# Performance work log

Measured on AMD Instinct MI355X. Metric: run time of the kernel, lower is better.

The kernel has to match this reference:

```python
import jax, jax.numpy as jnp
import numpy as np

B, Q, K, D, H = 2, 1024, 4096, 1024, 16
DH = D // H
LN_EPS = 1e-5


def setup_inputs() -> dict:
    key = jax.random.key(0)
    ks = jax.random.split(key, 10)
    queries = jax.random.normal(ks[0], (B, Q, D), jnp.float32)
    keys = jax.random.normal(ks[1], (B, K, D), jnp.float32)
    values = jax.random.normal(ks[2], (B, K, D), jnp.float32)
    # 128 words of 8 query tokens each: boundaries 0,8,...,1024 (sorted, unique)
    word_boundaries = jnp.arange(0, Q + 1, 8, dtype=jnp.int32)  # [129]
    # monotone map from query positions to char/key positions in [0, K]
    char_boundaries = jnp.sort(jax.random.randint(ks[3], (Q,), 0, K + 1, dtype=jnp.int32))
    s = 0.02
    ln_gamma = jnp.ones((D,), jnp.float32)
    ln_beta = jnp.zeros((D,), jnp.float32)
    in_proj_w = jax.random.normal(ks[4], (3 * D, D), jnp.float32) * s
    in_proj_b = jnp.zeros((3 * D,), jnp.float32)
    out_w = jax.random.normal(ks[5], (D, D), jnp.float32) * s
    out_b = jnp.zeros((D,), jnp.float32)
    return dict(queries=queries, keys=keys, values=values,
                word_boundaries=word_boundaries, char_boundaries=char_boundaries,
                ln_gamma=ln_gamma, ln_beta=ln_beta,
                in_proj_w=in_proj_w, in_proj_b=in_proj_b,
                out_w=out_w, out_b=out_b)


def char_aware_mask(wb, cb, q_len, k_len):
    """Vectorized version of the per-word python loop.
    Float mask of 0/1 (PyTorch ADDS a float attn_mask to the scores)."""
    ws, we = wb[:-1], wb[1:]                     # word start/end in query coords [nW]
    nW = ws.shape[0]
    cs = cb[ws]                                  # char span start per word
    ce = cb[we - 1]                              # char span end per word
    q = jnp.arange(q_len)
    i = jnp.clip(jnp.searchsorted(wb, q, side='right') - 1, 0, nW - 1)  # word id per query row
    valid = (q >= ws[i]) & (q < we[i])           # rows actually written by the loop
    j = jnp.arange(k_len)[None, :]               # [1, K]
    in_char = (j >= cs[i][:, None]) & (j < ce[i][:, None])
    # prev word: keys [wb[i-1], wb[i]) (query-coord indices used on key axis, as in source)
    ps = ws[jnp.maximum(i - 1, 0)]
    in_prev = (i > 0)[:, None] & (j >= ps[:, None]) & (j < ws[i][:, None])
    # next word: keys [wb[i+1], wb[i+2])
    ns = we[i]
    ne = wb[jnp.minimum(i + 2, nW)]
    in_next = (i < nW - 1)[:, None] & (j >= ns[:, None]) & (j < ne[:, None])
    return (valid[:, None] & (in_char | in_prev | in_next)).astype(jnp.float32)


def reference(queries, keys, values, word_boundaries, char_boundaries,
              ln_gamma, ln_beta, in_proj_w, in_proj_b, out_w, out_b):
    b, q_len, d = queries.shape
    k_len = keys.shape[1]
    mask = char_aware_mask(word_boundaries, char_boundaries, q_len, k_len)  # [Q, K]
    # LayerNorm(queries)
    mu = jnp.mean(queries, axis=-1, keepdims=True)
    var = jnp.var(queries, axis=-1, keepdims=True)
    x = (queries - mu) * jax.lax.rsqrt(var + LN_EPS) * ln_gamma + ln_beta
    # MultiheadAttention(x, keys, values, attn_mask=mask) -- float mask added to logits
    wq, wk, wv = jnp.split(in_proj_w, 3, axis=0)
    bq, bk, bv = jnp.split(in_proj_b, 3)
    qh = (x @ wq.T + bq).reshape(b, q_len, H, DH)
    kh = (keys @ wk.T + bk).reshape(b, k_len, H, DH)
    vh = (values @ wv.T + bv).reshape(b, k_len, H, DH)
    scale = 1.0 / jnp.sqrt(jnp.asarray(DH, queries.dtype))
    scores = jnp.einsum('bqhd,bkhd->bhqk', qh * scale, kh) + mask[None, None]
    attn = jax.nn.softmax(scores, axis=-1)
    ctx = jnp.einsum('bhqk,bkhd->bqhd', attn, vh).reshape(b, q_len, d)
    out = ctx @ out_w.T + out_b
    # residual; dropout is identity at inference
    return queries + out
```

## Files before the change

### kernel.cpp

```cpp
#include <hip/hip_runtime.h>
#include <hip/hip_bf16.h>


typedef __attribute__((ext_vector_type(8))) short bf16x8;
typedef __attribute__((ext_vector_type(4))) float f32x4;
typedef __attribute__((ext_vector_type(16))) float f32x16;

#define L2E 1.44269504088896341f
#define CSCALE (0.125f * L2E)
#define NSPLIT 4

__device__ __forceinline__ short f2bf(float f) {
  __hip_bfloat16 h = __float2bfloat16(f);
  return reinterpret_cast<short&>(h);
}

__device__ __forceinline__ unsigned cvtpk(float a, float b) {
  unsigned r;
  asm("v_cvt_pk_bf16_f32 %0, %1, %2" : "=v"(r) : "v"(a), "v"(b));
  return r;
}

__device__ __forceinline__ float fexp2(float x) {
#if __has_builtin(__builtin_amdgcn_exp2f)
  return __builtin_amdgcn_exp2f(x);
#else
  float r;
  asm("v_exp_f32 %0, %1" : "=v"(r) : "v"(x));
  return r;
#endif
}

__device__ __forceinline__ void halfswap(unsigned a, unsigned b, unsigned& x, unsigned& y) {
#if __has_builtin(__builtin_amdgcn_permlane32_swap)
  auto r = __builtin_amdgcn_permlane32_swap(a, b, false, false);
  x = (unsigned)r[0];
  y = (unsigned)r[1];
#else
  unsigned ca = (unsigned)__shfl_xor((int)a, 32);
  unsigned cb = (unsigned)__shfl_xor((int)b, 32);
  bool h = ((threadIdx.x & 63) >> 5) != 0;
  x = h ? cb : a;
  y = h ? b : ca;
#endif
}

__device__ __forceinline__ void gload16(const void* g, void* l) {
  __builtin_amdgcn_global_load_lds(
      (const __attribute__((address_space(1))) void*)g,
      (__attribute__((address_space(3))) void*)l, 16, 0, 0);
}

__device__ __forceinline__ void bar() { __builtin_amdgcn_s_barrier(); }

template <int N>
__device__ __forceinline__ void vmbar() {
  if constexpr (N == 8)
    asm volatile("s_waitcnt vmcnt(8)" ::: "memory");
  else
    asm volatile("s_waitcnt vmcnt(0)" ::: "memory");
  __builtin_amdgcn_s_barrier();
}

__device__ __forceinline__ void lgkm0() {
  asm volatile("s_waitcnt lgkmcnt(0)" ::: "memory");
  __builtin_amdgcn_sched_barrier(0);
}

__device__ __forceinline__ void ivcalc(int q, const int* __restrict__ wb,
                                       const int* __restrict__ cb, int* p) {
  int cnt = 0;
  for (int k = 0; k < 129; ++k) cnt += (wb[k] <= q) ? 1 : 0;
  int i = cnt - 1;
  i = i < 0 ? 0 : (i > 127 ? 127 : i);
  bool valid = (q >= wb[i]) && (q < wb[i + 1]);
  p[0] = p[1] = p[2] = p[3] = p[4] = p[5] = 0;
  if (valid) {
    p[0] = cb[wb[i]];
    p[1] = cb[wb[i + 1] - 1];
    if (i > 0) { p[2] = wb[i - 1]; p[3] = wb[i]; }
    if (i < 127) { p[4] = wb[i + 1]; p[5] = wb[(i + 2 <= 128) ? i + 2 : 128]; }
  }
}

__device__ __forceinline__ unsigned inrange3(int key, const int* p) {
  bool m = (key >= p[0] && key < p[1]) || (key >= p[2] && key < p[3]) ||
           (key >= p[4] && key < p[5]);
  return m ? 1u : 0u;
}

__global__ __launch_bounds__(256) void prep_kernel(const float* __restrict__ w,
                                                   const float* __restrict__ o,
                                                   short* __restrict__ dw,
                                                   short* __restrict__ dof,
                                                   const float* __restrict__ x,
                                                   const float* __restrict__ gamma,
                                                   const float* __restrict__ beta,
                                                   short* __restrict__ xout,
                                                   const int* __restrict__ wb,
                                                   const int* __restrict__ cb,
                                                   uint4* __restrict__ pmf,
                                                   const float* __restrict__ keys,
                                                   const float* __restrict__ values,
                                                   short* __restrict__ kbf,
                                                   short* __restrict__ vbf) {
  const int blk = blockIdx.x;
  const int t = threadIdx.x;
  if (blk < 2048) {
    int base = blk * 256 + t;
#pragma unroll
    for (int i = 0; i < 10; ++i) {
      long f = (long)base + (long)i * 524288;
      const float* s;
      short* d;
      if (f < 786432) {
        long e = f * 4;
        s = w + e; d = dw + e;
      } else if (f < 1048576) {
        long e = (f - 786432) * 4;
        s = o + e; d = dof + e;
      } else if (f < 3145728) {
        long e = (f - 1048576) * 4;
        s = keys + e; d = kbf + e;
      } else {
        long e = (f - 3145728) * 4;
        s = values + e; d = vbf + e;
      }
      float4 xv = *(const float4*)s;
      uint2 r;
      r.x = cvtpk(xv.x, xv.y);
      r.y = cvtpk(xv.z, xv.w);
      *(uint2*)d = r;
    }
  } else if (blk < 4096) {
    const int row = blk - 2048;
    float4 v = ((const float4*)(x + (size_t)row * 1024))[t];
    float s = v.x + v.y + v.z + v.w;
    float ss = v.x * v.x + v.y * v.y + v.z * v.z + v.w * v.w;
#pragma unroll
    for (int d = 32; d; d >>= 1) { s += __shfl_xor(s, d); ss += __shfl_xor(ss, d); }
    __shared__ float red[8];
    int wv2 = t >> 6, lane = t & 63;
    if (lane == 0) { red[wv2] = s; red[4 + wv2] = ss; }
    __syncthreads();
    s = red[0] + red[1] + red[2] + red[3];
    ss = red[4] + red[5] + red[6] + red[7];
    float mean = s * (1.0f / 1024.0f);
    float var = ss * (1.0f / 1024.0f) - mean * mean;
    float rstd = rsqrtf(var + 1e-5f);
    float4 g = ((const float4*)gamma)[t];
    float4 b = ((const float4*)beta)[t];
    uint2 oo;
    oo.x = cvtpk((v.x - mean) * rstd * g.x + b.x, (v.y - mean) * rstd * g.y + b.y);
    oo.y = cvtpk((v.z - mean) * rstd * g.z + b.z, (v.w - mean) * rstd * g.w + b.w);
    ((uint2*)(xout + (size_t)row * 1024))[t] = oo;
  } else {
    __shared__ int ivs[16][6];
    int mb = blk - 4096;
    if (t < 16) {
      int wg = (mb * 4 + (t >> 2)) & 31;
      int q = wg * 32 + (t & 3) * 8;
      ivcalc(q, wb, cb, ivs[t]);
    }
    __syncthreads();
    int idx = mb * 256 + t;
    int lane = idx & 63;
    int g4 = t >> 6;
    int tt = idx >> 11;
    int l31 = lane & 31, hi = lane >> 5;
    uint4 oo = {0u, 0u, 0u, 0u};
    if (!hi) {
      const int* p0 = ivs[g4 * 4 + 0];
      const int* p1 = ivs[g4 * 4 + 1];
      const int* p2 = ivs[g4 * 4 + 2];
      const int* p3 = ivs[g4 * 4 + 3];
      int key0 = tt * 64 + l31, key1 = key0 + 32;
      unsigned b0 = inrange3(key0, p0), b1 = inrange3(key0, p1);
      unsigned b2 = inrange3(key0, p2), b3 = inrange3(key0, p3);
      oo.x = (b0 | (b1 << 16)) * 0x3F80u;
      oo.y = (b2 | (b3 << 16)) * 0x3F80u;
      b0 = inrange3(key1, p0); b1 = inrange3(key1, p1);
      b2 = inrange3(key1, p2); b3 = inrange3(key1, p3);
      oo.z = (b0 | (b1 << 16)) * 0x3F80u;
      oo.w = (b2 | (b3 << 16)) * 0x3F80u;
    }
    pmf[idx] = oo;
  }
}

__device__ __forceinline__ void kv256_body(short* lds, const short* __restrict__ Agl,
                                           const short* __restrict__ Bgl,
                                           const float* __restrict__ bias,
                                           short* __restrict__ Cout, int mode,
                                           int bx, int by) {
  const int tid = (int)threadIdx.x;
  const int lane = tid & 63;
  const int w = tid >> 6;
  const int wm = w >> 2, wn = w & 3;
  const int l16 = lane & 15, lhi = lane >> 4;
  const int gc8 = (lane & 7) ^ (lane >> 3);
  const int lr = lane >> 3;
  const int rsw = (l16 & 7) << 4;
  const int m0 = bx * 256, n0 = by * 256;

  f32x4 acc[8][4];
#pragma unroll
  for (int i = 0; i < 8; ++i)
#pragma unroll
    for (int j = 0; j < 4; ++j) acc[i][j] = f32x4{0.f, 0.f, 0.f, 0.f};

  auto SU = [&](int k, int unit) {
    const int k0 = k * 64;
    short* base = lds + (k & 1) * 32768;
#pragma unroll
    for (int j = 0; j < 2; ++j) {
      int i = w * 2 + j;
      int ch;
      bool isA;
      if (unit == 1)      { ch = (i < 8) ? i : i + 8;       isA = true; }
      else if (unit == 4) { ch = 8 + ((i < 8) ? i : i + 8); isA = true; }
      else if (unit == 2) { ch = (i >> 2) * 8 + (i & 3);    isA = false; }
      else                { ch = 4 + (i >> 2) * 8 + (i & 3); isA = false; }
      const short* g = isA ? (Agl + (size_t)(m0 + ch * 8 + lr) * 1024 + k0 + gc8 * 8)
                           : (Bgl + (size_t)(n0 + ch * 8 + lr) * 1024 + k0 + gc8 * 8);
      gload16(g, base + (isA ? 0 : 16384) + ch * 512);
    }
  };

  bf16x8 af[4][2], b0[2][2], b1[2][2];
  auto LDA = [&](int bsel, int qm) {
    const char* cA = (const char*)(lds + bsel * 32768);
#pragma unroll
    for (int mt = 0; mt < 4; ++mt)
#pragma unroll
      for (int kk = 0; kk < 2; ++kk) {
        int row = wm * 128 + qm * 64 + mt * 16 + l16;
        af[mt][kk] = *(const bf16x8*)(cA + row * 128 + ((kk * 64 + lhi * 16) ^ rsw));
      }
  };
  auto LDB = [&](int bsel, int qn, bf16x8 (&bf)[2][2]) {
    const char* cB = (const char*)(lds + bsel * 32768) + 32768;
#pragma unroll
    for (int nt = 0; nt < 2; ++nt)
#pragma unroll
      for (int kk = 0; kk < 2; ++kk) {
        int row = wn * 64 + qn * 32 + nt * 16 + l16;
        bf[nt][kk] = *(const bf16x8*)(cB + row * 128 + ((kk * 64 + lhi * 16) ^ rsw));
      }
  };
  auto MM = [&](int qm, int qn, bf16x8 (&bf)[2][2]) {
    __builtin_amdgcn_s_setprio(1);
#pragma unroll
    for (int kk = 0; kk < 2; ++kk)
#pragma unroll
      for (int mt = 0; mt < 4; ++mt)
#pragma unroll
        for (int nt = 0; nt < 2; ++nt)
          acc[qm * 4 + mt][qn * 2 + nt] = __builtin_amdgcn_mfma_f32_16x16x32_bf16(
              af[mt][kk], bf[nt][kk], acc[qm * 4 + mt][qn * 2 + nt], 0, 0, 0);
    __builtin_amdgcn_s_setprio(0);
  };

  SU(0, 1); SU(0, 2); SU(0, 3); SU(0, 4);
  SU(1, 1); SU(1, 2); SU(1, 3); SU(1, 4);
  vmbar<8>();

#pragma unroll 2
  for (int k = 0; k < 14; ++k) {
    const int bs = k & 1;
    LDA(bs, 0); LDB(bs, 0, b0);
    lgkm0(); MM(0, 0, b0); bar();
    LDB(bs, 1, b1); SU(k + 2, 1);
    lgkm0(); MM(0, 1, b1); bar();
    LDA(bs, 1); SU(k + 2, 2);
    lgkm0(); MM(1, 0, b0); bar();
    SU(k + 2, 3); SU(k + 2, 4);
    MM(1, 1, b1);
    vmbar<8>();
  }
  {
    LDA(0, 0); LDB(0, 0, b0);
    lgkm0(); MM(0, 0, b0);
    LDB(0, 1, b1);
    lgkm0(); MM(0, 1, b1);
    LDA(0, 1);
    lgkm0(); MM(1, 0, b0);
    MM(1, 1, b1);
    vmbar<0>();
  }
  {
    LDA(1, 0); LDB(1, 0, b0);
    lgkm0(); MM(0, 0, b0);
    LDB(1, 1, b1);
    lgkm0(); MM(0, 1, b1);
    LDA(1, 1);
    lgkm0(); MM(1, 0, b0);
    MM(1, 1, b1);
  }

#pragma unroll
  for (int mt = 0; mt < 8; ++mt)
#pragma unroll
    for (int nt = 0; nt < 4; ++nt) {
      int n = n0 + wn * 64 + nt * 16 + l16;
#pragma unroll
      for (int r = 0; r < 4; ++r) {
        int m = m0 + wm * 128 + mt * 16 + lhi * 4 + r;
        float v = acc[mt][nt][r];
        if (mode == 0) {
          int bb = m >> 12, key = m & 4095;
          int hh = n >> 6, dhl = n & 63;
          Cout[((size_t)((bb * 16 + hh) * 4096 + key)) * 64 + dhl] = f2bf(v + bias[n]);
        } else {
          int bb = n >> 12, key = n & 4095;
          Cout[((size_t)(bb * 1024 + m)) * 4096 + key] = f2bf(v + bias[m]);
        }
      }
    }
}

__device__ __forceinline__ void gemmQO_body(short* lA, short* lB,
                                            const short* __restrict__ A,
                                            const short* __restrict__ W,
                                            const float* __restrict__ bias,
                                            const float* __restrict__ resid,
                                            void* __restrict__ Cout, int mode,
                                            float scale, int bxi, int byi) {
  const int lane = threadIdx.x & 63;
  const int w = threadIdx.x >> 6;
  const int m0 = bxi * 64;
  const int n0 = byi * 128;
  const int wm = w >> 2, wn = w & 3;
  const int l16 = lane & 15, lhi = lane >> 4;

  const int gc8 = (lane & 7) ^ (lane >> 3);
  const int lr = lane >> 3;
  const int rsw = (l16 & 7) << 4;

  f32x4 zero = {0.f, 0.f, 0.f, 0.f};
  f32x4 acc[2][2];
#pragma unroll
  for (int i = 0; i < 2; ++i)
#pragma unroll
    for (int j = 0; j < 2; ++j) acc[i][j] = zero;

  for (int k0 = 0; k0 < 1024; k0 += 64) {
    __syncthreads();
#pragma unroll
    for (int j = 0; j < 3; ++j) {
      int c = w * 3 + j;
      if (c < 8)
        gload16(A + (size_t)(m0 + c * 8 + lr) * 1024 + k0 + gc8 * 8, &lA[c * 512]);
      else
        gload16(W + (size_t)(n0 + (c - 8) * 8 + lr) * 1024 + k0 + gc8 * 8,
                &lB[(c - 8) * 512]);
    }
    __syncthreads();
    bf16x8 af[2][2], bfr[2][2];
#pragma unroll
    for (int mt = 0; mt < 2; ++mt)
#pragma unroll
      for (int kk = 0; kk < 2; ++kk)
        af[mt][kk] = *(const bf16x8*)((const char*)lA + (wm * 32 + mt * 16 + l16) * 128 +
                                      ((kk * 64 + lhi * 16) ^ rsw));
#pragma unroll
    for (int nt = 0; nt < 2; ++nt)
#pragma unroll
      for (int kk = 0; kk < 2; ++kk)
        bfr[nt][kk] = *(const bf16x8*)((const char*)lB + (wn * 32 + nt * 16 + l16) * 128 +
                                       ((kk * 64 + lhi * 16) ^ rsw));
#pragma unroll
    for (int kk = 0; kk < 2; ++kk)
#pragma unroll
      for (int mt = 0; mt < 2; ++mt)
#pragma unroll
        for (int nt = 0; nt < 2; ++nt)
          acc[mt][nt] = __builtin_amdgcn_mfma_f32_16x16x32_bf16(af[mt][kk], bfr[nt][kk],
                                                                acc[mt][nt], 0, 0, 0);
  }

#pragma unroll
  for (int mt = 0; mt < 2; ++mt)
#pragma unroll
    for (int nt = 0; nt < 2; ++nt) {
      int col = n0 + wn * 32 + nt * 16 + l16;
      float bs = bias[col];
#pragma unroll
      for (int r = 0; r < 4; ++r) {
        int row = m0 + wm * 32 + mt * 16 + lhi * 4 + r;
        float v = acc[mt][nt][r] + bs;
        if (mode == 0) {
          ((short*)Cout)[(size_t)row * 1024 + col] = f2bf(v * scale);
        } else {
          size_t idx = (size_t)row * 1024 + col;
          ((float*)Cout)[idx] = v + resid[idx];
        }
      }
    }
}

__global__ __launch_bounds__(512, 2) void megaGemm_kernel(const short* __restrict__ kbf,
                                                          const short* __restrict__ wk,
                                                          const float* __restrict__ kbias,
                                                          const short* __restrict__ wv,
                                                          const short* __restrict__ vbf,
                                                          const float* __restrict__ vbias,
                                                          short* __restrict__ khp,
                                                          short* __restrict__ vhT,
                                                          const short* __restrict__ xb,
                                                          const short* __restrict__ wq,
                                                          const float* __restrict__ qbias,
                                                          short* __restrict__ qhb) {
  __shared__ __attribute__((aligned(16))) short lds[65536];
  int id = blockIdx.x;
  if (id < 128) {
    kv256_body(lds, kbf, wk, kbias, khp, 0, id & 31, id >> 5);
  } else if (id < 256) {
    int i2 = id & 127;
    kv256_body(lds, wv, vbf, vbias, vhT, 1, i2 >> 5, i2 & 31);
  } else {
    int i2 = id - 256;
    gemmQO_body(lds, lds + 4096, xb, wq, qbias, nullptr, qhb, 0, CSCALE, i2 & 31, i2 >> 5);
  }
}

__global__ __launch_bounds__(512, 4) void gemmQO_kernel(const short* __restrict__ A,
                                                        const short* __restrict__ W,
                                                        const float* __restrict__ bias,
                                                        const float* __restrict__ resid,
                                                        void* __restrict__ Cout, int mode,
                                                        float scale) {
  __shared__ __attribute__((aligned(16))) short lA[4096];
  __shared__ __attribute__((aligned(16))) short lB[8192];
  gemmQO_body(lA, lB, A, W, bias, resid, Cout, mode, scale, blockIdx.x, blockIdx.y);
}

__global__ __launch_bounds__(256, 4) void attn15_kernel(const short* __restrict__ qh,
                                                        const short* __restrict__ khp,
                                                        const short* __restrict__ vtp,
                                                        const uint4* __restrict__ pmf,
                                                        short* __restrict__ pacc,
                                                        float* __restrict__ pml) {
  const int tid = threadIdx.x;
  const int lane = tid & 63;
  const int w = tid >> 6;
  const int l31 = lane & 31;
  const int hi = lane >> 5;
  const int id = blockIdx.x;
  const int qb = id >> 7;
  const int g = id & 127;
  const int bh = g >> 2;
  const int ks = g & 3;
  const int b = bh >> 4, h = bh & 15;

  __shared__ __attribute__((aligned(16))) short sK[2][4096];
  __shared__ __attribute__((aligned(16))) short sV[2][4096];

  const int wq0 = qb * 128 + w * 32;
  const int qrow = wq0 + l31;
  bf16x8 qf0, qf1, qf2, qf3;
  {
    const short* qp = qh + ((size_t)(b * 1024 + qrow)) * 1024 + h * 64 + hi * 8;
    qf0 = *(const bf16x8*)(qp);
    qf1 = *(const bf16x8*)(qp + 16);
    qf2 = *(const bf16x8*)(qp + 32);
    qf3 = *(const bf16x8*)(qp + 48);
  }

  bf16x8 bmv;
  {
    union { unsigned u[4]; bf16x8 v; } t;
    t.u[0] = t.u[1] = t.u[2] = t.u[3] = 0;
    int lj = l31 >> 3;
    unsigned val = 0x3FB9u << (16 * (lj & 1));
    if (!hi) t.u[lj >> 1] = val;
    bmv = t.v;
  }

  f32x16 fzero;
#pragma unroll
  for (int i = 0; i < 16; ++i) fzero[i] = 0.f;

  const int kchunk = ks * 1024;
  const int sub = (lane & 7) ^ (lane >> 3);
  const int r8 = lane >> 3;
  const size_t kbase_g = ((size_t)bh * 4096 + kchunk) * 64;
  const size_t vbase_g = ((size_t)bh * 64) * 4096 + (size_t)kchunk;
  const uint4* pmfp = pmf + ((size_t)(ks * 16) * 32 + qb * 4 + w) * 64 + lane;

  f32x16 acc0, acc1;
#pragma unroll
  for (int i = 0; i < 16; ++i) { acc0[i] = 0.f; acc1[i] = 0.f; }
  float rs = 0.f;

  const int koff_swz = ((lane & 7) ^ ((lane >> 3) & 3)) << 4;

  auto STAGE = [&](int buf, int t) {
    int kt = t * 64;
#pragma unroll
    for (int q2 = 0; q2 < 2; ++q2) {
      int ch = w * 2 + q2;
      int sub2 = sub ^ (ch & 3);
      gload16(khp + kbase_g + (size_t)(kt + ch * 8 + r8) * 64 + sub2 * 8,
              (short*)sK[buf] + ch * 512);
      gload16(vtp + vbase_g + (size_t)(ch * 8 + r8) * 4096 + kt + sub2 * 8,
              (short*)sV[buf] + ch * 512);
    }
  };

  auto HALF = [&](int buf, unsigned mlo, unsigned mhi, int rowb, bf16x8& paA, bf16x8& paB) {
    bf16x8 am;
    {
      union { unsigned u[4]; bf16x8 v; } f;
      f.u[0] = mlo; f.u[1] = mhi; f.u[2] = 0; f.u[3] = 0;
      am = f.v;
    }
    __builtin_amdgcn_s_setprio(1);
    f32x16 ss = __builtin_amdgcn_mfma_f32_32x32x16_bf16(am, bmv, fzero, 0, 0, 0);
#pragma unroll
    for (int c = 0; c < 4; ++c) {
      int off = (c * 32 + hi * 16) ^ koff_swz;
      bf16x8 k0 = *(const bf16x8*)((const char*)sK[buf] + (rowb + l31) * 128 + off);
      bf16x8 qc = (c == 0) ? qf0 : (c == 1) ? qf1 : (c == 2) ? qf2 : qf3;
      ss = __builtin_amdgcn_mfma_f32_32x32x16_bf16(k0, qc, ss, 0, 0, 0);
    }
    __builtin_amdgcn_s_setprio(0);
#pragma unroll
    for (int r = 0; r < 16; ++r) ss[r] = fexp2(ss[r]);
    {
      float t0 = ss[0] + ss[1], t1 = ss[2] + ss[3], t2 = ss[4] + ss[5], t3 = ss[6] + ss[7];
      float t4 = ss[8] + ss[9], t5 = ss[10] + ss[11], t6 = ss[12] + ss[13],
            t7 = ss[14] + ss[15];
      rs += ((t0 + t1) + (t2 + t3)) + ((t4 + t5) + (t6 + t7));
    }
    unsigned a01 = cvtpk(ss[0], ss[1]), a23 = cvtpk(ss[2], ss[3]);
    unsigned a45 = cvtpk(ss[4], ss[5]), a67 = cvtpk(ss[6], ss[7]);
    unsigned a89 = cvtpk(ss[8], ss[9]), aAB = cvtpk(ss[10], ss[11]);
    unsigned aCD = cvtpk(ss[12], ss[13]), aEF = cvtpk(ss[14], ss[15]);
    union { unsigned u[4]; bf16x8 v; } f;
    halfswap(a01, a45, f.u[0], f.u[2]);
    halfswap(a23, a67, f.u[1], f.u[3]);
    paA = f.v;
    halfswap(a89, aCD, f.u[0], f.u[2]);
    halfswap(aAB, aEF, f.u[1], f.u[3]);
    paB = f.v;
  };

  uint4 mf_cur = pmfp[0];
  uint4 mf_next = mf_cur;
  STAGE(0, 0);
  __syncthreads();
  int buf = 0;

  for (int t = 0; t < 16; ++t) {
    if (t < 15) {
      STAGE(buf ^ 1, t + 1);
      mf_next = pmfp[(size_t)(t + 1) * 2048];
    }

    bf16x8 pa0, pa1, pa2, pa3;
    HALF(buf, mf_cur.x, mf_cur.y, 0, pa0, pa1);
    HALF(buf, mf_cur.z, mf_cur.w, 32, pa2, pa3);

    __builtin_amdgcn_s_setprio(1);
#pragma unroll
    for (int kb16 = 0; kb16 < 4; ++kb16) {
      int off = (kb16 * 32 + hi * 16) ^ koff_swz;
      bf16x8 v0 = *(const bf16x8*)((const char*)sV[buf] + l31 * 128 + off);
      bf16x8 v1 = *(const bf16x8*)((const char*)sV[buf] + (32 + l31) * 128 + off);
      bf16x8 pa = (kb16 == 0) ? pa0 : (kb16 == 1) ? pa1 : (kb16 == 2) ? pa2 : pa3;
      acc0 = __builtin_amdgcn_mfma_f32_32x32x16_bf16(pa, v0, acc0, 0, 0, 0);
      acc1 = __builtin_amdgcn_mfma_f32_32x32x16_bf16(pa, v1, acc1, 0, 0, 0);
    }
    __builtin_amdgcn_s_setprio(0);
    __syncthreads();
    buf ^= 1;
    mf_cur = mf_next;
  }

  short* paccp = pacc + (((size_t)ks * 32 + bh) * 1024) * 64;
#pragma unroll
  for (int r = 0; r < 16; r += 2) {
    int q0 = wq0 + ((r & 3) + 8 * (r >> 2)) + 4 * hi;
    int q1 = wq0 + (((r + 1) & 3) + 8 * ((r + 1) >> 2)) + 4 * hi;
    unsigned u0 = cvtpk(acc0[r], acc0[r + 1]);
    unsigned u1 = cvtpk(acc1[r], acc1[r + 1]);
    paccp[(size_t)q0 * 64 + l31] = (short)(u0 & 0xffffu);
    paccp[(size_t)q1 * 64 + l31] = (short)(u0 >> 16);
    paccp[(size_t)q0 * 64 + 32 + l31] = (short)(u1 & 0xffffu);
    paccp[(size_t)q1 * 64 + 32 + l31] = (short)(u1 >> 16);
  }
  rs += __shfl_xor(rs, 32);
  if (hi == 0) {
    float* mlp = pml + ((size_t)ks * 32 + bh) * 1024;
    mlp[wq0 + l31] = rs;
  }
}

__global__ __launch_bounds__(256) void combine_kernel(const short* __restrict__ pacc,
                                                      const float* __restrict__ pml,
                                                      short* __restrict__ ctx) {
  int idx = blockIdx.x * 256 + threadIdx.x;
  int dh8 = idx & 7;
  int row = idx >> 3;
  int bh = row >> 10, q = row & 1023;
  float L = 0.f;
  float o0 = 0.f, o1 = 0.f, o2 = 0.f, o3 = 0.f, o4 = 0.f, o5 = 0.f, o6 = 0.f, o7 = 0.f;
#pragma unroll
  for (int k = 0; k < NSPLIT; ++k) {
    L += pml[((size_t)k * 32 + bh) * 1024 + q];
    uint4 u = *(const uint4*)&pacc[(((size_t)k * 32 + bh) * 1024 + q) * 64 + dh8 * 8];
    unsigned t0 = u.x << 16, t1 = u.x & 0xffff0000u;
    unsigned t2 = u.y << 16, t3 = u.y & 0xffff0000u;
    unsigned t4 = u.z << 16, t5 = u.z & 0xffff0000u;
    unsigned t6 = u.w << 16, t7 = u.w & 0xffff0000u;
    o0 += reinterpret_cast<float&>(t0);
    o1 += reinterpret_cast<float&>(t1);
    o2 += reinterpret_cast<float&>(t2);
    o3 += reinterpret_cast<float&>(t3);
    o4 += reinterpret_cast<float&>(t4);
    o5 += reinterpret_cast<float&>(t5);
    o6 += reinterpret_cast<float&>(t6);
    o7 += reinterpret_cast<float&>(t7);
  }
  float inv = 1.0f / L;
  uint4 st;
  st.x = cvtpk(o0 * inv, o1 * inv);
  st.y = cvtpk(o2 * inv, o3 * inv);
  st.z = cvtpk(o4 * inv, o5 * inv);
  st.w = cvtpk(o6 * inv, o7 * inv);
  int b = bh >> 4, h = bh & 15;
  *(uint4*)&ctx[((size_t)(b * 1024 + q)) * 1024 + h * 64 + dh8 * 8] = st;
}

extern "C" void kernel_launch(void* const* d_in, const int* in_sizes, int n_in,
                              void* d_out, int out_size, void* d_ws, size_t ws_size,
                              hipStream_t stream) {
  const float* queries = (const float*)d_in[0];
  const float* keys    = (const float*)d_in[1];
  const float* values  = (const float*)d_in[2];
  const int*   wb      = (const int*)d_in[3];
  const int*   cb      = (const int*)d_in[4];
  const float* gamma   = (const float*)d_in[5];
  const float* beta    = (const float*)d_in[6];
  const float* ipw     = (const float*)d_in[7];
  const float* ipb     = (const float*)d_in[8];
  const float* ow      = (const float*)d_in[9];
  const float* ob      = (const float*)d_in[10];
  float* out = (float*)d_out;

  char* p = (char*)d_ws;
  short* xb  = (short*)p; p += (size_t)2048 * 1024 * 2;
  short* kb  = (short*)p; p += (size_t)8192 * 1024 * 2;
  short* vb  = (short*)p; p += (size_t)8192 * 1024 * 2;
  short* wpb = (short*)p; p += (size_t)3072 * 1024 * 2;
  short* owb = (short*)p; p += (size_t)1024 * 1024 * 2;
  short* qhb = (short*)p; p += (size_t)2048 * 1024 * 2;
  short* khp = (short*)p; p += (size_t)8192 * 1024 * 2;
  short* vhT = (short*)p; p += (size_t)8192 * 1024 * 2;
  short* ctx = (short*)p; p += (size_t)2048 * 1024 * 2;
  uint4* pmf = (uint4*)p; p += (size_t)64 * 32 * 64 * 16;
  if ((size_t)(p - (char*)d_ws) > ws_size) return;

  short* pacc = kb;
  float* pml  = (float*)wpb;

  prep_kernel<<<4608, 256, 0, stream>>>(ipw, ow, wpb, owb, queries, gamma, beta, xb,
                                        wb, cb, pmf, keys, values, kb, vb);

  megaGemm_kernel<<<512, 512, 0, stream>>>(kb, wpb + 1048576, ipb + 1024,
                                           wpb + 2097152, vb, ipb + 2048,
                                           khp, vhT, xb, wpb, ipb, qhb);

  attn15_kernel<<<1024, 256, 0, stream>>>(qhb, khp, vhT, pmf, pacc, pml);
  combine_kernel<<<1024, 256, 0, stream>>>(pacc, pml, ctx);

  gemmQO_kernel<<<dim3(32, 8), 512, 0, stream>>>(ctx, owb, ob, queries, out, 2, 1.f);
}
```

Measured before the change: 141.9 us.

## Fuse split-K attention combine into output projection GEMM A-tile load

Removes the separate combine kernel and the ctx buffer by merging the four split-K partial accumulators and normalizing by the summed row sums directly while staging the A tile into LDS in the output-projection GEMM. This saves one launch and a write plus read of the bf16 context tensor. In exchange, each of the 8 column-blocks recomputes the combine for its rows, so partial results are read 8 times. The A-tile loads are now synchronous compute rather than async gloads, which may stall the GEMM loop.

```diff
diff --git a/kernel.cpp b/kernel.cpp
--- a/kernel.cpp
+++ b/kernel.cpp
@@ -424,15 +424,112 @@
   }
 }
 
-__global__ __launch_bounds__(512, 4) void gemmQO_kernel(const short* __restrict__ A,
-                                                        const short* __restrict__ W,
-                                                        const float* __restrict__ bias,
-                                                        const float* __restrict__ resid,
-                                                        void* __restrict__ Cout, int mode,
-                                                        float scale) {
+__global__ __launch_bounds__(512, 4) void gemmOut_kernel(const short* __restrict__ pacc,
+                                                         const float* __restrict__ pml,
+                                                         const short* __restrict__ W,
+                                                         const float* __restrict__ bias,
+                                                         const float* __restrict__ resid,
+                                                         float* __restrict__ out) {
   __shared__ __attribute__((aligned(16))) short lA[4096];
   __shared__ __attribute__((aligned(16))) short lB[8192];
-  gemmQO_body(lA, lB, A, W, bias, resid, Cout, mode, scale, blockIdx.x, blockIdx.y);
+  const int lane = threadIdx.x & 63;
+  const int w = threadIdx.x >> 6;
+  const int m0 = blockIdx.x * 64;
+  const int n0 = blockIdx.y * 128;
+  const int wm = w >> 2, wn = w & 3;
+  const int l16 = lane & 15, lhi = lane >> 4;
+
+  const int gc8 = (lane & 7) ^ (lane >> 3);
+  const int lr = lane >> 3;
+  const int rsw = (l16 & 7) << 4;
+
+  f32x4 zero = {0.f, 0.f, 0.f, 0.f};
+  f32x4 acc[2][2];
+#pragma unroll
+  for (int i = 0; i < 2; ++i)
+#pragma unroll
+    for (int j = 0; j < 2; ++j) acc[i][j] = zero;
+
+  for (int k0 = 0; k0 < 1024; k0 += 64) {
+    __syncthreads();
+#pragma unroll
+    for (int j = 0; j < 3; ++j) {
+      int c = w * 3 + j;
+      if (c < 8) {
+        int row = m0 + c * 8 + lr;
+        int q = row & 1023, b = row >> 10;
+        int bh = b * 16 + (k0 >> 6);
+        int dh0 = gc8 * 8;
+        float L = 0.f;
+        float o0 = 0.f, o1 = 0.f, o2 = 0.f, o3 = 0.f;
+        float o4 = 0.f, o5 = 0.f, o6 = 0.f, o7 = 0.f;
+#pragma unroll
+        for (int ks = 0; ks < NSPLIT; ++ks) {
+          size_t base = ((size_t)ks * 32 + bh) * 1024 + q;
+          L += pml[base];
+          uint4 u = *(const uint4*)&pacc[base * 64 + dh0];
+          unsigned t0 = u.x << 16, t1 = u.x & 0xffff0000u;
+          unsigned t2 = u.y << 16, t3 = u.y & 0xffff0000u;
+          unsigned t4 = u.z << 16, t5 = u.z & 0xffff0000u;
+          unsigned t6 = u.w << 16, t7 = u.w & 0xffff0000u;
+          o0 += reinterpret_cast<float&>(t0);
+          o1 += reinterpret_cast<float&>(t1);
+          o2 += reinterpret_cast<float&>(t2);
+          o3 += reinterpret_cast<float&>(t3);
+          o4 += reinterpret_cast<float&>(t4);
+          o5 += reinterpret_cast<float&>(t5);
+          o6 += reinterpret_cast<float&>(t6);
+          o7 += reinterpret_cast<float&>(t7);
+        }
+        float inv = 1.0f / L;
+        uint4 st;
+        st.x = cvtpk(o0 * inv, o1 * inv);
+        st.y = cvtpk(o2 * inv, o3 * inv);
+        st.z = cvtpk(o4 * inv, o5 * inv);
+        st.w = cvtpk(o6 * inv, o7 * inv);
+        *(uint4*)&lA[c * 512 + lane * 8] = st;
+      } else {
+        gload16(W + (size_t)(n0 + (c - 8) * 8 + lr) * 1024 + k0 + gc8 * 8,
+                &lB[(c - 8) * 512]);
+      }
+    }
+    __syncthreads();
+    bf16x8 af[2][2], bfr[2][2];
+#pragma unroll
+    for (int mt = 0; mt < 2; ++mt)
+#pragma unroll
+      for (int kk = 0; kk < 2; ++kk)
+        af[mt][kk] = *(const bf16x8*)((const char*)lA + (wm * 32 + mt * 16 + l16) * 128 +
+                                      ((kk * 64 + lhi * 16) ^ rsw));
+#pragma unroll
+    for (int nt = 0; nt < 2; ++nt)
+#pragma unroll
+      for (int kk = 0; kk < 2; ++kk)
+        bfr[nt][kk] = *(const bf16x8*)((const char*)lB + (wn * 32 + nt * 16 + l16) * 128 +
+                                       ((kk * 64 + lhi * 16) ^ rsw));
+#pragma unroll
+    for (int kk = 0; kk < 2; ++kk)
+#pragma unroll
+      for (int mt = 0; mt < 2; ++mt)
+#pragma unroll
+        for (int nt = 0; nt < 2; ++nt)
+          acc[mt][nt] = __builtin_amdgcn_mfma_f32_16x16x32_bf16(af[mt][kk], bfr[nt][kk],
+                                                                acc[mt][nt], 0, 0, 0);
+  }
+
+#pragma unroll
+  for (int mt = 0; mt < 2; ++mt)
+#pragma unroll
+    for (int nt = 0; nt < 2; ++nt) {
+      int col = n0 + wn * 32 + nt * 16 + l16;
+      float bs = bias[col];
+#pragma unroll
+      for (int r = 0; r < 4; ++r) {
+        int row = m0 + wm * 32 + mt * 16 + lhi * 4 + r;
+        size_t idx = (size_t)row * 1024 + col;
+        out[idx] = acc[mt][nt][r] + bs + resid[idx];
+      }
+    }
 }
 
 __global__ __launch_bounds__(256, 4) void attn15_kernel(const short* __restrict__ qh,
@@ -597,42 +694,6 @@
   }
 }
 
-__global__ __launch_bounds__(256) void combine_kernel(const short* __restrict__ pacc,
-                                                      const float* __restrict__ pml,
-                                                      short* __restrict__ ctx) {
-  int idx = blockIdx.x * 256 + threadIdx.x;
-  int dh8 = idx & 7;
-  int row = idx >> 3;
-  int bh = row >> 10, q = row & 1023;
-  float L = 0.f;
-  float o0 = 0.f, o1 = 0.f, o2 = 0.f, o3 = 0.f, o4 = 0.f, o5 = 0.f, o6 = 0.f, o7 = 0.f;
-#pragma unroll
-  for (int k = 0; k < NSPLIT; ++k) {
-    L += pml[((size_t)k * 32 + bh) * 1024 + q];
-    uint4 u = *(const uint4*)&pacc[(((size_t)k * 32 + bh) * 1024 + q) * 64 + dh8 * 8];
-    unsigned t0 = u.x << 16, t1 = u.x & 0xffff0000u;
-    unsigned t2 = u.y << 16, t3 = u.y & 0xffff0000u;
-    unsigned t4 = u.z << 16, t5 = u.z & 0xffff0000u;
-    unsigned t6 = u.w << 16, t7 = u.w & 0xffff0000u;
-    o0 += reinterpret_cast<float&>(t0);
-    o1 += reinterpret_cast<float&>(t1);
-    o2 += reinterpret_cast<float&>(t2);
-    o3 += reinterpret_cast<float&>(t3);
-    o4 += reinterpret_cast<float&>(t4);
-    o5 += reinterpret_cast<float&>(t5);
-    o6 += reinterpret_cast<float&>(t6);
-    o7 += reinterpret_cast<float&>(t7);
-  }
-  float inv = 1.0f / L;
-  uint4 st;
-  st.x = cvtpk(o0 * inv, o1 * inv);
-  st.y = cvtpk(o2 * inv, o3 * inv);
-  st.z = cvtpk(o4 * inv, o5 * inv);
-  st.w = cvtpk(o6 * inv, o7 * inv);
-  int b = bh >> 4, h = bh & 15;
-  *(uint4*)&ctx[((size_t)(b * 1024 + q)) * 1024 + h * 64 + dh8 * 8] = st;
-}
-
 extern "C" void kernel_launch(void* const* d_in, const int* in_sizes, int n_in,
                               void* d_out, int out_size, void* d_ws, size_t ws_size,
                               hipStream_t stream) {
@@ -658,7 +719,6 @@
   short* qhb = (short*)p; p += (size_t)2048 * 1024 * 2;
   short* khp = (short*)p; p += (size_t)8192 * 1024 * 2;
   short* vhT = (short*)p; p += (size_t)8192 * 1024 * 2;
-  short* ctx = (short*)p; p += (size_t)2048 * 1024 * 2;
   uint4* pmf = (uint4*)p; p += (size_t)64 * 32 * 64 * 16;
   if ((size_t)(p - (char*)d_ws) > ws_size) return;
 
@@ -673,7 +733,6 @@
                                            khp, vhT, xb, wpb, ipb, qhb);
 
   attn15_kernel<<<1024, 256, 0, stream>>>(qhb, khp, vhT, pmf, pacc, pml);
-  combine_kernel<<<1024, 256, 0, stream>>>(pacc, pml, ctx);
-
-  gemmQO_kernel<<<dim3(32, 8), 512, 0, stream>>>(ctx, owb, ob, queries, out, 2, 1.f);
-}
+
+  gemmOut_kernel<<<dim3(32, 8), 512, 0, stream>>>(pacc, pml, owb, ob, queries, out);
+}
```

After: 206.1 us. +45.3%, slower.
